# Kernel tuning notes

Hardware: AMD Instinct MI355X
Metric: run time of the kernel (lower is better)

The kernel has to match this reference:

```python
import jax, jax.numpy as jnp
import numpy as np

EPS = 1e-08
F_DIM = 512


def setup_inputs() -> dict:
    key = jax.random.key(0)
    ks = jax.random.split(key, 7)
    N, F = 50000, F_DIM
    q = jax.random.normal(ks[0], (N, 1, F), dtype=jnp.float32)
    mu = jax.random.normal(ks[1], (N, 3, F), dtype=jnp.float32)
    # Xavier-ish scaled params
    W_mix = jax.random.normal(ks[2], (2 * F, F), dtype=jnp.float32) * (1.0 / np.sqrt(F))
    W1 = jax.random.normal(ks[3], (F, 2 * F), dtype=jnp.float32) * (1.0 / np.sqrt(2 * F))
    b1 = jnp.zeros((F,), dtype=jnp.float32)
    W2 = jax.random.normal(ks[4], (3 * F, F), dtype=jnp.float32) * (1.0 / np.sqrt(F))
    b2 = jnp.zeros((3 * F,), dtype=jnp.float32)
    return {"q": q, "mu": mu, "W_mix": W_mix, "W1": W1, "b1": b1, "W2": W2, "b2": b2}


def reference(q, mu, W_mix, W1, b1, W2, b2):
    F = q.shape[-1]
    # mu_channel_mix: [N,3,F] @ [F,2F] -> [N,3,2F]
    mu_mix = jnp.einsum('ndf,gf->ndg', mu, W_mix)
    mu_V, mu_W = mu_mix[..., :F], mu_mix[..., F:]
    # vector norm over Cartesian axis -> [N,1,F]
    mu_Vn = jnp.sqrt(jnp.sum(mu_V * mu_V, axis=-2, keepdims=True) + EPS)
    ctx = jnp.concatenate([q, mu_Vn], axis=-1)  # [N,1,2F]
    h = jax.nn.silu(jnp.einsum('nsf,gf->nsg', ctx, W1) + b1)  # [N,1,F]
    x = jnp.einsum('nsf,gf->nsg', h, W2) + b2  # [N,1,3F]
    dq_intra = x[..., :F]
    dmu_intra = x[..., F:2 * F] * mu_W  # broadcast [N,1,F]*[N,3,F]
    dqmu_intra = x[..., 2 * F:] * jnp.sum(mu_V * mu_W, axis=1, keepdims=True)
    q_out = q + dq_intra + dqmu_intra
    mu_out = mu + dmu_intra
    return (q_out, mu_out)
```

## Files before the change

kernel.cpp:

```cpp
#include <hip/hip_runtime.h>
#include <stdint.h>

#define NN 50000
#define QWORDS 25600000

typedef __attribute__((ext_vector_type(8))) short bf16x8;
typedef __attribute__((ext_vector_type(4))) float f32x4;

__device__ __forceinline__ uint32_t f2bf(float x){
  uint32_t u = __builtin_bit_cast(uint32_t, x);
  u += 0x7FFFu + ((u >> 16) & 1u);
  return u >> 16;
}
__device__ __forceinline__ float bf2f(uint32_t b){
  uint32_t u = b << 16;
  return __builtin_bit_cast(float, u);
}
__device__ __forceinline__ void gload16(const uint16_t* g, uint16_t* l){
  __builtin_amdgcn_global_load_lds(
      (const __attribute__((address_space(1))) uint32_t*)g,
      (__attribute__((address_space(3))) uint32_t*)l, 16, 0, 0);
}
__device__ __forceinline__ f32x4 mfma16(bf16x8 a, bf16x8 b, f32x4 c){
  return __builtin_amdgcn_mfma_f32_16x16x32_bf16(a, b, c, 0, 0, 0);
}

#define FENCE() asm volatile("" ::: "memory")

__global__ void k_convert(const float* __restrict__ wmix, const float* __restrict__ w1,
                          const float* __restrict__ w2, uint16_t* __restrict__ dst){
  int i = blockIdx.x * 256 + threadIdx.x;
  int e = i << 2;
  const float* s; int o;
  if (e < 524288)       { s = wmix; o = e; }
  else if (e < 1048576) { s = w1;   o = e - 524288; }
  else                  { s = w2;   o = e - 1048576; }
  f32x4 v = *(const f32x4*)(s + o);
  uint2 pk;
  pk.x = f2bf(v[0]) | (f2bf(v[1]) << 16);
  pk.y = f2bf(v[2]) | (f2bf(v[3]) << 16);
  *(uint2*)(dst + e) = pk;
}

__global__ void k_convmu(const float* __restrict__ mu, uint16_t* __restrict__ dst){
  size_t i = (size_t)blockIdx.x * 256 + threadIdx.x;
  size_t e = i << 2;
  f32x4 v = *(const f32x4*)(mu + e);
  uint2 pk;
  pk.x = f2bf(v[0]) | (f2bf(v[1]) << 16);
  pk.y = f2bf(v[2]) | (f2bf(v[3]) << 16);
  *(uint2*)(dst + e) = pk;
}

__global__ __launch_bounds__(512, 4)
void k_gemm1(const float* __restrict__ mu, const uint16_t* __restrict__ wmixb,
             uint16_t* __restrict__ qh, float* __restrict__ muW){
  __shared__ uint16_t As[2][12288];
  __shared__ uint16_t Bs[2][8192];
  const int tid  = threadIdx.x;
  const int lane = tid & 63;
  const int w    = tid >> 6;
  const int wn   = w & 3;
  const int wf   = w >> 2;
  const int orig = blockIdx.x;
  const int j    = (orig & 7) * 782 + (orig >> 3);
  const int f0   = (j & 7) * 64;
  const int n0   = (j >> 3) * 64;
  const int lrow = tid >> 4;
  const int lcol = (tid & 15) * 4;

  f32x4 ar[6];
  auto A_LOAD = [&](int ks){
    const int k0 = ks * 64;
    #pragma unroll
    for (int p=0; p<6; ++p){
      int r = p*32 + lrow;
      int d = r >> 6, nrow = r & 63;
      int n = n0 + nrow;
      int g = (n < NN ? n : NN-1)*3 + d;
      ar[p] = *(const f32x4*)(mu + (size_t)g*512 + k0 + lcol);
    }
  };
  auto A_WRITE = [&](int buf){
    #pragma unroll
    for (int p=0; p<6; ++p){
      int r = p*32 + lrow;
      f32x4 v = ar[p];
      uint2 pk;
      pk.x = f2bf(v[0]) | (f2bf(v[1]) << 16);
      pk.y = f2bf(v[2]) | (f2bf(v[3]) << 16);
      *(uint2*)&As[buf][r*64 + (lcol ^ ((r&7)<<3))] = pk;
    }
  };
  auto B_ISSUE = [&](int ks, int buf){
    const int k0 = ks * 64;
    #pragma unroll
    for (int jj=0; jj<2; ++jj){
      int jb = w*2 + jj;
      int row = jb*8 + (lane>>3);
      int g = (row < 64) ? (f0 + row) : (448 + f0 + row);
      int srcc = ((lane&7) ^ ((lane>>3)&7)) * 8;
      gload16(wmixb + (size_t)g*512 + k0 + srcc, &Bs[buf][jb*512]);
    }
  };

  const f32x4 z4 = {0.f,0.f,0.f,0.f};
  f32x4 acc[3][4];
  #pragma unroll
  for (int d=0; d<3; ++d)
    #pragma unroll
    for (int nt=0; nt<4; ++nt) acc[d][nt] = z4;

  A_LOAD(0); B_ISSUE(0, 0); A_WRITE(0);
  for (int ks=0; ks<8; ++ks){
    const int cur = ks & 1;
    __syncthreads();
    if (ks < 7){ A_LOAD(ks+1); B_ISSUE(ks+1, cur^1); }
    #pragma unroll
    for (int kf=0; kf<2; ++kf){
      int kc = kf*32 + (lane>>4)*8;
      bf16x8 af[3];
      #pragma unroll
      for (int d=0; d<3; ++d){
        int r = d*64 + wn*16 + (lane&15);
        af[d] = *(const bf16x8*)&As[cur][r*64 + (kc ^ ((r&7)<<3))];
      }
      #pragma unroll
      for (int nt=0; nt<4; ++nt){
        int ntg = wf*2 + (nt&1) + (nt>>1)*4;
        int rr = ntg*16 + (lane&15);
        bf16x8 bf = *(const bf16x8*)&Bs[cur][rr*64 + (kc ^ ((rr&7)<<3))];
        #pragma unroll
        for (int d=0; d<3; ++d)
          acc[d][nt] = mfma16(bf, af[d], acc[d][nt]);
      }
    }
    if (ks < 7) A_WRITE(cur^1);
  }

  const int rb4 = (lane >> 4) * 4;
  const int nthr = n0 + wn*16 + (lane & 15);
  if (nthr < NN){
    #pragma unroll
    for (int c=0; c<2; ++c){
      int f = f0 + (wf*2 + c)*16 + rb4;
      uint2 pkv, pkd; f32x4 u0v, u1v, u2v;
      uint32_t vb[4], db[4];
      #pragma unroll
      for (int p=0; p<4; ++p){
        float v0 = acc[0][c][p],   v1 = acc[1][c][p],   v2 = acc[2][c][p];
        float u0 = acc[0][c+2][p], u1 = acc[1][c+2][p], u2 = acc[2][c+2][p];
        float vn = sqrtf(v0*v0 + v1*v1 + v2*v2 + 1e-8f);
        float dt = v0*u0 + v1*u1 + v2*u2;
        vb[p] = f2bf(vn); db[p] = f2bf(dt);
        u0v[p] = u0; u1v[p] = u1; u2v[p] = u2;
      }
      pkv.x = vb[0] | (vb[1] << 16); pkv.y = vb[2] | (vb[3] << 16);
      pkd.x = db[0] | (db[1] << 16); pkd.y = db[2] | (db[3] << 16);
      *(uint2*)(qh + (size_t)nthr*1024 + f)       = pkv;
      *(uint2*)(qh + (size_t)nthr*1024 + 512 + f) = pkd;
      size_t mb = (size_t)nthr*1536 + f;
      *(f32x4*)(muW + mb)        = u0v;
      *(f32x4*)(muW + mb + 512)  = u1v;
      *(f32x4*)(muW + mb + 1024) = u2v;
    }
  }
}

__global__ __launch_bounds__(512, 4)
void k_gemm1b(const uint16_t* __restrict__ mu16, const uint16_t* __restrict__ wmixb,
              uint16_t* __restrict__ qh, float* __restrict__ muW){
  __shared__ uint16_t As[2][12288];
  __shared__ uint16_t Bs[2][8192];
  const int tid  = threadIdx.x;
  const int lane = tid & 63;
  const int w    = tid >> 6;
  const int wn   = w & 3;
  const int wf   = w >> 2;
  const int orig = blockIdx.x;
  const int j    = (orig & 7) * 782 + (orig >> 3);
  const int f0   = (j & 7) * 64;
  const int n0   = (j >> 3) * 64;

  auto A_ISSUE = [&](int ks, int buf){
    const int k0 = ks * 64;
    #pragma unroll
    for (int jj=0; jj<3; ++jj){
      int jb = w*3 + jj;
      int rr = jb*8 + (lane>>3);
      int d = rr >> 6, nrow = rr & 63;
      int n = n0 + nrow;
      int g = (n < NN ? n : NN-1)*3 + d;
      int srcc = ((lane&7) ^ ((lane>>3)&7)) * 8;
      gload16(mu16 + (size_t)g*512 + k0 + srcc, &As[buf][jb*512]);
    }
  };
  auto B_ISSUE = [&](int ks, int buf){
    const int k0 = ks * 64;
    #pragma unroll
    for (int jj=0; jj<2; ++jj){
      int jb = w*2 + jj;
      int row = jb*8 + (lane>>3);
      int g = (row < 64) ? (f0 + row) : (448 + f0 + row);
      int srcc = ((lane&7) ^ ((lane>>3)&7)) * 8;
      gload16(wmixb + (size_t)g*512 + k0 + srcc, &Bs[buf][jb*512]);
    }
  };

  const f32x4 z4 = {0.f,0.f,0.f,0.f};
  f32x4 acc[3][4];
  #pragma unroll
  for (int d=0; d<3; ++d)
    #pragma unroll
    for (int nt=0; nt<4; ++nt) acc[d][nt] = z4;

  A_ISSUE(0, 0); B_ISSUE(0, 0);
  for (int ks=0; ks<8; ++ks){
    const int cur = ks & 1;
    __syncthreads();
    if (ks < 7){ A_ISSUE(ks+1, cur^1); B_ISSUE(ks+1, cur^1); }
    #pragma unroll
    for (int kf=0; kf<2; ++kf){
      int kc = kf*32 + (lane>>4)*8;
      bf16x8 af[3];
      #pragma unroll
      for (int d=0; d<3; ++d){
        int r = d*64 + wn*16 + (lane&15);
        af[d] = *(const bf16x8*)&As[cur][r*64 + (kc ^ ((r&7)<<3))];
      }
      #pragma unroll
      for (int nt=0; nt<4; ++nt){
        int ntg = wf*2 + (nt&1) + (nt>>1)*4;
        int rr = ntg*16 + (lane&15);
        bf16x8 bf = *(const bf16x8*)&Bs[cur][rr*64 + (kc ^ ((rr&7)<<3))];
        #pragma unroll
        for (int d=0; d<3; ++d)
          acc[d][nt] = mfma16(bf, af[d], acc[d][nt]);
      }
    }
  }

  const int rb4 = (lane >> 4) * 4;
  const int nthr = n0 + wn*16 + (lane & 15);
  if (nthr < NN){
    #pragma unroll
    for (int c=0; c<2; ++c){
      int f = f0 + (wf*2 + c)*16 + rb4;
      uint2 pkv, pkd; f32x4 u0v, u1v, u2v;
      uint32_t vb[4], db[4];
      #pragma unroll
      for (int p=0; p<4; ++p){
        float v0 = acc[0][c][p],   v1 = acc[1][c][p],   v2 = acc[2][c][p];
        float u0 = acc[0][c+2][p], u1 = acc[1][c+2][p], u2 = acc[2][c+2][p];
        float vn = sqrtf(v0*v0 + v1*v1 + v2*v2 + 1e-8f);
        float dt = v0*u0 + v1*u1 + v2*u2;
        vb[p] = f2bf(vn); db[p] = f2bf(dt);
        u0v[p] = u0; u1v[p] = u1; u2v[p] = u2;
      }
      pkv.x = vb[0] | (vb[1] << 16); pkv.y = vb[2] | (vb[3] << 16);
      pkd.x = db[0] | (db[1] << 16); pkd.y = db[2] | (db[3] << 16);
      *(uint2*)(qh + (size_t)nthr*1024 + f)       = pkv;
      *(uint2*)(qh + (size_t)nthr*1024 + 512 + f) = pkd;
      size_t mb = (size_t)nthr*1536 + f;
      *(f32x4*)(muW + mb)        = u0v;
      *(f32x4*)(muW + mb + 512)  = u1v;
      *(f32x4*)(muW + mb + 1024) = u2v;
    }
  }
}

__global__ __launch_bounds__(512, 4)
void k_gemm2(const float* __restrict__ q, const uint16_t* __restrict__ w1b,
             const float* __restrict__ b1, uint16_t* __restrict__ qh){
  __shared__ uint16_t A2[2][2048];
  __shared__ uint16_t B2[2][16384];
  const int tid  = threadIdx.x;
  const int lane = tid & 63;
  const int w    = tid >> 6;
  const int wm   = w >> 2;
  const int wn   = w & 3;
  const int n0   = blockIdx.x * 64;

  f32x4 qa;
  auto QA_LOAD = [&](int s){
    int k0 = s*32;
    int row = tid >> 3, ch = tid & 7;
    int nc = (n0 + row < NN) ? n0 + row : NN-1;
    qa = *(const f32x4*)(q + (size_t)nc*512 + k0 + ch*4);
  };
  auto QA_WRITE = [&](int buf){
    int row = tid >> 3, ch = tid & 7;
    uint2 pk;
    pk.x = f2bf(qa[0]) | (f2bf(qa[1]) << 16);
    pk.y = f2bf(qa[2]) | (f2bf(qa[3]) << 16);
    *(uint2*)&A2[buf][row*32 + (((ch>>1) ^ (row&3))<<3) + (ch&1)*4] = pk;
  };
  auto VA_ISSUE = [&](int s, int buf){
    if (w < 4){
      int k0v = (s-16)*32;
      int row = w*16 + (lane>>2);
      int nc = (n0 + row < NN) ? n0 + row : NN-1;
      int srcch = (lane&3) ^ (row&3);
      gload16(qh + (size_t)nc*1024 + k0v + srcch*8, &A2[buf][w*512]);
    }
  };
  auto B_ISSUE = [&](int s, int buf){
    int k0 = s*32;
    #pragma unroll
    for (int jj=0; jj<4; ++jj){
      int j = w*4 + jj;
      int row = j*16 + (lane>>2);
      int srcch = (lane&3) ^ (row&3);
      gload16(w1b + (size_t)row*1024 + k0 + srcch*8, &B2[buf][j*512]);
    }
  };

  const f32x4 z4 = {0.f,0.f,0.f,0.f};
  f32x4 acc2[2][8];
  #pragma unroll
  for (int mt=0; mt<2; ++mt)
    #pragma unroll
    for (int nt=0; nt<8; ++nt) acc2[mt][nt] = z4;

  QA_LOAD(0); B_ISSUE(0, 0); QA_WRITE(0);
  for (int s=0; s<32; ++s){
    const int cur = s & 1;
    __syncthreads();
    if (s < 31){
      if (s+1 < 16) QA_LOAD(s+1); else VA_ISSUE(s+1, cur^1);
      B_ISSUE(s+1, cur^1);
    }
    {
      int kc = (lane>>4)*8;
      bf16x8 a[2];
      #pragma unroll
      for (int mt=0; mt<2; ++mt){
        int r = wm*32 + mt*16 + (lane&15);
        a[mt] = *(const bf16x8*)&A2[cur][r*32 + (kc ^ ((r&3)<<3))];
      }
      #pragma unroll
      for (int nt=0; nt<8; ++nt){
        int rr = wn*128 + nt*16 + (lane&15);
        bf16x8 b = *(const bf16x8*)&B2[cur][rr*32 + (kc ^ ((rr&3)<<3))];
        acc2[0][nt] = mfma16(a[0], b, acc2[0][nt]);
        acc2[1][nt] = mfma16(a[1], b, acc2[1][nt]);
      }
    }
    if (s < 31 && s+1 < 16) QA_WRITE(cur^1);
  }

  const int rb4 = (lane >> 4) * 4;
  #pragma unroll
  for (int nt=0; nt<8; ++nt){
    int col = wn*128 + nt*16 + (lane&15);
    float bb = b1[col];
    #pragma unroll
    for (int mt=0; mt<2; ++mt)
      #pragma unroll
      for (int j=0; j<4; ++j){
        int n = n0 + wm*32 + mt*16 + rb4 + j;
        if (n < NN){
          float x = acc2[mt][nt][j] + bb;
          float sv = x / (1.f + __expf(-x));
          qh[(size_t)n*1024 + col] = (uint16_t)f2bf(sv);
        }
      }
  }
}

__global__ __launch_bounds__(512, 4)
void k_gemm3(const float* __restrict__ q, const float* __restrict__ mu,
             const uint16_t* __restrict__ w2b, const float* __restrict__ b2,
             float* __restrict__ dout){
  __shared__ uint16_t Hs[32*512];
  __shared__ uint16_t B3[2][12288];
  const int tid  = threadIdx.x;
  const int lane = tid & 63;
  const int w    = tid >> 6;
  const int wm   = w >> 2;
  const int wn   = w & 3;
  const int n0   = blockIdx.x * 32;
  const uint16_t* qh = (const uint16_t*)dout;
  float* mout = dout + (size_t)QWORDS;
  const int l15 = lane & 15;
  const int rb4 = (lane >> 4) * 4;
  const f32x4 z4 = {0.f,0.f,0.f,0.f};

  #pragma unroll
  for (int i=0; i<4; ++i){
    int row = w*4 + i;
    int nc = (n0 + row < NN) ? n0 + row : NN-1;
    gload16(qh + (size_t)nc*1024 + (size_t)((lane ^ (row&7))*8), &Hs[row*512]);
  }

  auto B_ISSUE = [&](int it, int ks, uint16_t* slot){
    #pragma unroll
    for (int jj=0; jj<3; ++jj){
      int j = w*3 + jj;
      int rr = j*8 + (lane>>3);
      int s3 = rr >> 6, fi = rr & 63;
      int g = s3*512 + it*64 + fi;
      gload16(w2b + (size_t)g*512 + ks*64 + ((lane&7) ^ (rr&7))*8, slot + j*512);
    }
  };
  B_ISSUE(0, 0, B3[0]);

  const int nthr = n0 + wm*16 + l15;
  const int nc   = nthr < NN ? nthr : NN-1;

  f32x4 qv, bbv[3], muv[3], mwv[3];
  float dtv[4];
  int   fb = 0;
  f32x4 acc3[3];

#define K3_MFMA(KS) do{ \
    const uint16_t* bsl = B3[(KS)&1]; \
    __builtin_amdgcn_s_setprio(1); \
    _Pragma("unroll") \
    for (int kf=0; kf<2; ++kf){ \
      int r = wm*16 + l15; \
      int ch = ((KS)*8 + kf*4 + (lane>>4)) ^ (r&7); \
      bf16x8 a = *(const bf16x8*)&Hs[r*512 + ch*8]; \
      _Pragma("unroll") \
      for (int s3=0; s3<3; ++s3){ \
        int rr = s3*64 + wn*16 + l15; \
        int chb = (kf*4 + (lane>>4)) ^ (rr&7); \
        bf16x8 b = *(const bf16x8*)&bsl[rr*64 + chb*8]; \
        acc3[s3] = mfma16(b, a, acc3[s3]); \
      } \
    } \
    __builtin_amdgcn_s_setprio(0); \
  } while(0)

  #pragma unroll 1
  for (int it=0; it<8; ++it){
    if (it) { asm volatile("s_waitcnt vmcnt(4)" ::: "memory"); }
    else    { asm volatile("s_waitcnt vmcnt(0)" ::: "memory"); }
    __builtin_amdgcn_s_barrier();
    B_ISSUE(it, 1, B3[1]);
    FENCE();
    {
      #pragma unroll
      for (int s3=0; s3<3; ++s3) acc3[s3] = z4;
      fb = it*64 + wn*16 + rb4;
      bbv[0] = *(const f32x4*)(b2 + fb);
      bbv[1] = *(const f32x4*)(b2 + 512 + fb);
      bbv[2] = *(const f32x4*)(b2 + 1024 + fb);
      uint2 du = *(const uint2*)(qh + (size_t)nc*1024 + 512 + fb);
      dtv[0] = bf2f(du.x & 0xffff); dtv[1] = bf2f(du.x >> 16);
      dtv[2] = bf2f(du.y & 0xffff); dtv[3] = bf2f(du.y >> 16);
      qv = *(const f32x4*)(q + (size_t)nc*512 + fb);
    }
    FENCE();
    K3_MFMA(0);

    asm volatile("s_waitcnt vmcnt(5)" ::: "memory");
    __builtin_amdgcn_s_barrier();
    B_ISSUE(it, 2, B3[0]);
    FENCE();
    {
      size_t mb = (size_t)nc*1536 + fb;
      muv[0] = *(const f32x4*)(mu + mb);
      muv[1] = *(const f32x4*)(mu + mb + 512);
      muv[2] = *(const f32x4*)(mu + mb + 1024);
    }
    FENCE();
    K3_MFMA(1);

    asm volatile("s_waitcnt vmcnt(3)" ::: "memory");
    __builtin_amdgcn_s_barrier();
    B_ISSUE(it, 3, B3[1]);
    FENCE();
    {
      size_t mb = (size_t)nc*1536 + fb;
      mwv[0] = *(const f32x4*)(mout + mb);
      mwv[1] = *(const f32x4*)(mout + mb + 512);
      mwv[2] = *(const f32x4*)(mout + mb + 1024);
    }
    FENCE();
    K3_MFMA(2);

    asm volatile("s_waitcnt vmcnt(3)" ::: "memory");
    __builtin_amdgcn_s_barrier();
    B_ISSUE(it, 4, B3[0]);
    FENCE();
    K3_MFMA(3);

    asm volatile("s_waitcnt vmcnt(0)" ::: "memory");
    __builtin_amdgcn_s_barrier();
    B_ISSUE(it, 5, B3[1]);
    FENCE();
    K3_MFMA(4);

    asm volatile("s_waitcnt vmcnt(0)" ::: "memory");
    __builtin_amdgcn_s_barrier();
    B_ISSUE(it, 6, B3[0]);
    FENCE();
    K3_MFMA(5);

    asm volatile("s_waitcnt vmcnt(0)" ::: "memory");
    __builtin_amdgcn_s_barrier();
    B_ISSUE(it, 7, B3[1]);
    FENCE();
    K3_MFMA(6);

    asm volatile("s_waitcnt vmcnt(0)" ::: "memory");
    __builtin_amdgcn_s_barrier();
    if (it < 7) B_ISSUE(it+1, 0, B3[0]);
    FENCE();
    K3_MFMA(7);
    if (nthr < NN){
      f32x4 qo, m0, m1, m2;
      #pragma unroll
      for (int p=0; p<4; ++p){
        float x0 = acc3[0][p] + bbv[0][p];
        float x1 = acc3[1][p] + bbv[1][p];
        float x2 = acc3[2][p] + bbv[2][p];
        qo[p] = qv[p] + x0 + x2*dtv[p];
        m0[p] = muv[0][p] + x1*mwv[0][p];
        m1[p] = muv[1][p] + x1*mwv[1][p];
        m2[p] = muv[2][p] + x1*mwv[2][p];
      }
      *(f32x4*)(dout + (size_t)nthr*512 + fb) = qo;
      size_t mb = (size_t)nthr*1536 + fb;
      *(f32x4*)(mout + mb)        = m0;
      *(f32x4*)(mout + mb + 512)  = m1;
      *(f32x4*)(mout + mb + 1024) = m2;
    }
  }
#undef K3_MFMA
}

extern "C" void kernel_launch(void* const* d_in, const int* in_sizes, int n_in,
                              void* d_out, int out_size, void* d_ws, size_t ws_size,
                              hipStream_t stream){
  (void)in_sizes; (void)n_in; (void)out_size;
  const float* q    = (const float*)d_in[0];
  const float* mu   = (const float*)d_in[1];
  const float* wmix = (const float*)d_in[2];
  const float* w1   = (const float*)d_in[3];
  const float* b1   = (const float*)d_in[4];
  const float* w2   = (const float*)d_in[5];
  const float* b2   = (const float*)d_in[6];
  uint16_t* wb = (uint16_t*)d_ws;
  float* dout = (float*)d_out;

  hipLaunchKernelGGL(k_convert, dim3(1792), dim3(256), 0, stream, wmix, w1, w2, wb);

  const size_t need = ((size_t)1835008 + (size_t)NN*1536) * 2;
  if (ws_size >= need){
    uint16_t* mu16 = wb + 1835008;
    hipLaunchKernelGGL(k_convmu, dim3(75000), dim3(256), 0, stream, mu, mu16);
    hipLaunchKernelGGL(k_gemm1b, dim3(6256), dim3(512), 0, stream,
                       mu16, wb, (uint16_t*)d_out, dout + (size_t)QWORDS);
  } else {
    hipLaunchKernelGGL(k_gemm1, dim3(6256), dim3(512), 0, stream,
                       mu, wb, (uint16_t*)d_out, dout + (size_t)QWORDS);
  }

  hipLaunchKernelGGL(k_gemm2, dim3(782), dim3(512), 0, stream,
                     q, wb + 524288, b1, (uint16_t*)d_out);
  hipLaunchKernelGGL(k_gemm3, dim3(1563), dim3(512), 0, stream,
                     q, mu, wb + 1048576, b2, dout);
}
```

Measured before the change: 916.3 us.

## Fuse mu bf16 conversion into gemm1 and store mu_W intermediate as bf16

```diff
diff --git a/kernel.cpp b/kernel.cpp
--- a/kernel.cpp
+++ b/kernel.cpp
@@ -36,16 +36,6 @@
   else if (e < 1048576) { s = w1;   o = e - 524288; }
   else                  { s = w2;   o = e - 1048576; }
   f32x4 v = *(const f32x4*)(s + o);
-  uint2 pk;
-  pk.x = f2bf(v[0]) | (f2bf(v[1]) << 16);
-  pk.y = f2bf(v[2]) | (f2bf(v[3]) << 16);
-  *(uint2*)(dst + e) = pk;
-}
-
-__global__ void k_convmu(const float* __restrict__ mu, uint16_t* __restrict__ dst){
-  size_t i = (size_t)blockIdx.x * 256 + threadIdx.x;
-  size_t e = i << 2;
-  f32x4 v = *(const f32x4*)(mu + e);
   uint2 pk;
   pk.x = f2bf(v[0]) | (f2bf(v[1]) << 16);
   pk.y = f2bf(v[2]) | (f2bf(v[3]) << 16);
@@ -168,8 +158,8 @@
 }
 
 __global__ __launch_bounds__(512, 4)
-void k_gemm1b(const uint16_t* __restrict__ mu16, const uint16_t* __restrict__ wmixb,
-              uint16_t* __restrict__ qh, float* __restrict__ muW){
+void k_gemm1b(const float* __restrict__ mu, const uint16_t* __restrict__ wmixb,
+              uint16_t* __restrict__ qh, uint16_t* __restrict__ mw16){
   __shared__ uint16_t As[2][12288];
   __shared__ uint16_t Bs[2][8192];
   const int tid  = threadIdx.x;
@@ -181,18 +171,30 @@
   const int j    = (orig & 7) * 782 + (orig >> 3);
   const int f0   = (j & 7) * 64;
   const int n0   = (j >> 3) * 64;
-
-  auto A_ISSUE = [&](int ks, int buf){
+  const int lrow = tid >> 4;
+  const int lcol = (tid & 15) * 4;
+
+  f32x4 ar[6];
+  auto A_LOAD = [&](int ks){
     const int k0 = ks * 64;
     #pragma unroll
-    for (int jj=0; jj<3; ++jj){
-      int jb = w*3 + jj;
-      int rr = jb*8 + (lane>>3);
-      int d = rr >> 6, nrow = rr & 63;
+    for (int p=0; p<6; ++p){
+      int r = p*32 + lrow;
+      int d = r >> 6, nrow = r & 63;
       int n = n0 + nrow;
       int g = (n < NN ? n : NN-1)*3 + d;
-      int srcc = ((lane&7) ^ ((lane>>3)&7)) * 8;
-      gload16(mu16 + (size_t)g*512 + k0 + srcc, &As[buf][jb*512]);
+      ar[p] = *(const f32x4*)(mu + (size_t)g*512 + k0 + lcol);
+    }
+  };
+  auto A_WRITE = [&](int buf){
+    #pragma unroll
+    for (int p=0; p<6; ++p){
+      int r = p*32 + lrow;
+      f32x4 v = ar[p];
+      uint2 pk;
+      pk.x = f2bf(v[0]) | (f2bf(v[1]) << 16);
+      pk.y = f2bf(v[2]) | (f2bf(v[3]) << 16);
+      *(uint2*)&As[buf][r*64 + (lcol ^ ((r&7)<<3))] = pk;
     }
   };
   auto B_ISSUE = [&](int ks, int buf){
@@ -214,11 +216,11 @@
     #pragma unroll
     for (int nt=0; nt<4; ++nt) acc[d][nt] = z4;
 
-  A_ISSUE(0, 0); B_ISSUE(0, 0);
+  A_LOAD(0); B_ISSUE(0, 0); A_WRITE(0);
   for (int ks=0; ks<8; ++ks){
     const int cur = ks & 1;
     __syncthreads();
-    if (ks < 7){ A_ISSUE(ks+1, cur^1); B_ISSUE(ks+1, cur^1); }
+    if (ks < 7){ A_LOAD(ks+1); B_ISSUE(ks+1, cur^1); }
     #pragma unroll
     for (int kf=0; kf<2; ++kf){
       int kc = kf*32 + (lane>>4)*8;
@@ -238,6 +240,7 @@
           acc[d][nt] = mfma16(bf, af[d], acc[d][nt]);
       }
     }
+    if (ks < 7) A_WRITE(cur^1);
   }
 
   const int rb4 = (lane >> 4) * 4;
@@ -246,8 +249,8 @@
     #pragma unroll
     for (int c=0; c<2; ++c){
       int f = f0 + (wf*2 + c)*16 + rb4;
-      uint2 pkv, pkd; f32x4 u0v, u1v, u2v;
-      uint32_t vb[4], db[4];
+      uint2 pkv, pkd, pw0, pw1, pw2;
+      uint32_t vb[4], db[4], w0[4], w1[4], w2[4];
       #pragma unroll
       for (int p=0; p<4; ++p){
         float v0 = acc[0][c][p],   v1 = acc[1][c][p],   v2 = acc[2][c][p];
@@ -255,16 +258,19 @@
         float vn = sqrtf(v0*v0 + v1*v1 + v2*v2 + 1e-8f);
         float dt = v0*u0 + v1*u1 + v2*u2;
         vb[p] = f2bf(vn); db[p] = f2bf(dt);
-        u0v[p] = u0; u1v[p] = u1; u2v[p] = u2;
+        w0[p] = f2bf(u0); w1[p] = f2bf(u1); w2[p] = f2bf(u2);
       }
       pkv.x = vb[0] | (vb[1] << 16); pkv.y = vb[2] | (vb[3] << 16);
       pkd.x = db[0] | (db[1] << 16); pkd.y = db[2] | (db[3] << 16);
+      pw0.x = w0[0] | (w0[1] << 16); pw0.y = w0[2] | (w0[3] << 16);
+      pw1.x = w1[0] | (w1[1] << 16); pw1.y = w1[2] | (w1[3] << 16);
+      pw2.x = w2[0] | (w2[1] << 16); pw2.y = w2[2] | (w2[3] << 16);
       *(uint2*)(qh + (size_t)nthr*1024 + f)       = pkv;
       *(uint2*)(qh + (size_t)nthr*1024 + 512 + f) = pkd;
       size_t mb = (size_t)nthr*1536 + f;
-      *(f32x4*)(muW + mb)        = u0v;
-      *(f32x4*)(muW + mb + 512)  = u1v;
-      *(f32x4*)(muW + mb + 1024) = u2v;
+      *(uint2*)(mw16 + mb)        = pw0;
+      *(uint2*)(mw16 + mb + 512)  = pw1;
+      *(uint2*)(mw16 + mb + 1024) = pw2;
     }
   }
 }
@@ -368,50 +374,127 @@
   }
 }
 
-__global__ __launch_bounds__(512, 4)
-void k_gemm3(const float* __restrict__ q, const float* __restrict__ mu,
-             const uint16_t* __restrict__ w2b, const float* __restrict__ b2,
-             float* __restrict__ dout){
-  __shared__ uint16_t Hs[32*512];
-  __shared__ uint16_t B3[2][12288];
-  const int tid  = threadIdx.x;
-  const int lane = tid & 63;
-  const int w    = tid >> 6;
-  const int wm   = w >> 2;
-  const int wn   = w & 3;
-  const int n0   = blockIdx.x * 32;
-  const uint16_t* qh = (const uint16_t*)dout;
-  float* mout = dout + (size_t)QWORDS;
-  const int l15 = lane & 15;
-  const int rb4 = (lane >> 4) * 4;
-  const f32x4 z4 = {0.f,0.f,0.f,0.f};
-
-  #pragma unroll
-  for (int i=0; i<4; ++i){
-    int row = w*4 + i;
-    int nc = (n0 + row < NN) ? n0 + row : NN-1;
-    gload16(qh + (size_t)nc*1024 + (size_t)((lane ^ (row&7))*8), &Hs[row*512]);
-  }
-
-  auto B_ISSUE = [&](int it, int ks, uint16_t* slot){
-    #pragma unroll
-    for (int jj=0; jj<3; ++jj){
-      int j = w*3 + jj;
-      int rr = j*8 + (lane>>3);
-      int s3 = rr >> 6, fi = rr & 63;
-      int g = s3*512 + it*64 + fi;
-      gload16(w2b + (size_t)g*512 + ks*64 + ((lane&7) ^ (rr&7))*8, slot + j*512);
-    }
-  };
-  B_ISSUE(0, 0, B3[0]);
-
-  const int nthr = n0 + wm*16 + l15;
-  const int nc   = nthr < NN ? nthr : NN-1;
-
-  f32x4 qv, bbv[3], muv[3], mwv[3];
-  float dtv[4];
-  int   fb = 0;
-  f32x4 acc3[3];
+#define K3_BODY(MW_LOAD_STMT)                                                  \
+  __shared__ uint16_t Hs[32*512];                                    \
+  __shared__ uint16_t B3[2][12288];                           \
+  const int tid  = threadIdx.x;                                                \
+  const int lane = tid & 63;                                                   \
+  const int w    = tid >> 6;                                                   \
+  const int wm   = w >> 2;                                                     \
+  const int wn   = w & 3;                                                      \
+  const int n0   = blockIdx.x * 32;                                            \
+  const uint16_t* qh = (const uint16_t*)dout;                                  \
+  float* mout = dout + (size_t)QWORDS;                                         \
+  const int l15 = lane & 15;                                                   \
+  const int rb4 = (lane >> 4) * 4;                                             \
+  const f32x4 z4 = {0.f,0.f,0.f,0.f};                                          \
+  _Pragma("unroll")                                                            \
+  for (int i=0; i<4; ++i){                                                     \
+    int row = w*4 + i;                                                         \
+    int nc2 = (n0 + row < NN) ? n0 + row : NN-1;                               \
+    gload16(qh + (size_t)nc2*1024 + (size_t)((lane ^ (row&7))*8), &Hs[row*512]);\
+  }                                                                            \
+  auto B_ISSUE = [&](int it, int ks, uint16_t* slot){                          \
+    _Pragma("unroll")                                                          \
+    for (int jj=0; jj<3; ++jj){                                                \
+      int jx = w*3 + jj;                                                       \
+      int rr = jx*8 + (lane>>3);                                               \
+      int s3 = rr >> 6, fi = rr & 63;                                          \
+      int g = s3*512 + it*64 + fi;                                             \
+      gload16(w2b + (size_t)g*512 + ks*64 + ((lane&7) ^ (rr&7))*8, slot + jx*512);\
+    }                                                                          \
+  };                                                                           \
+  B_ISSUE(0, 0, B3[0]);                                                        \
+  const int nthr = n0 + wm*16 + l15;                                           \
+  const int nc   = nthr < NN ? nthr : NN-1;                                    \
+  f32x4 qv, bbv[3], muv[3], mwv[3];                                            \
+  float dtv[4];                                                                \
+  int   fb = 0;                                                                \
+  f32x4 acc3[3];                                                               \
+  _Pragma("unroll 1")                                                          \
+  for (int it=0; it<8; ++it){                                                  \
+    if (it) { asm volatile("s_waitcnt vmcnt(4)" ::: "memory"); }               \
+    else    { asm volatile("s_waitcnt vmcnt(0)" ::: "memory"); }               \
+    __builtin_amdgcn_s_barrier();                                              \
+    B_ISSUE(it, 1, B3[1]);                                                     \
+    FENCE();                                                                   \
+    {                                                                          \
+      _Pragma("unroll")                                                        \
+      for (int s3=0; s3<3; ++s3) acc3[s3] = z4;                                \
+      fb = it*64 + wn*16 + rb4;                                                \
+      bbv[0] = *(const f32x4*)(b2 + fb);                                       \
+      bbv[1] = *(const f32x4*)(b2 + 512 + fb);                                 \
+      bbv[2] = *(const f32x4*)(b2 + 1024 + fb);                                \
+      uint2 du = *(const uint2*)(qh + (size_t)nc*1024 + 512 + fb);             \
+      dtv[0] = bf2f(du.x & 0xffff); dtv[1] = bf2f(du.x >> 16);                 \
+      dtv[2] = bf2f(du.y & 0xffff); dtv[3] = bf2f(du.y >> 16);                 \
+      qv = *(const f32x4*)(q + (size_t)nc*512 + fb);                           \
+    }                                                                          \
+    FENCE();                                                                   \
+    K3_MFMA(0);                                                                \
+    asm volatile("s_waitcnt vmcnt(5)" ::: "memory");                           \
+    __builtin_amdgcn_s_barrier();                                              \
+    B_ISSUE(it, 2, B3[0]);                                                     \
+    FENCE();                                                                   \
+    {                                                                          \
+      size_t mb = (size_t)nc*1536 + fb;                                        \
+      muv[0] = *(const f32x4*)(mu + mb);                                       \
+      muv[1] = *(const f32x4*)(mu + mb + 512);                                 \
+      muv[2] = *(const f32x4*)(mu + mb + 1024);                                \
+    }                                                                          \
+    FENCE();                                                                   \
+    K3_MFMA(1);                                                                \
+    asm volatile("s_waitcnt vmcnt(3)" ::: "memory");                           \
+    __builtin_amdgcn_s_barrier();                                              \
+    B_ISSUE(it, 3, B3[1]);                                                     \
+    FENCE();                                                                   \
+    { MW_LOAD_STMT }                                                           \
+    FENCE();                                                                   \
+    K3_MFMA(2);                                                                \
+    asm volatile("s_waitcnt vmcnt(3)" ::: "memory");                           \
+    __builtin_amdgcn_s_barrier();                                              \
+    B_ISSUE(it, 4, B3[0]);                                                     \
+    FENCE();                                                                   \
+    K3_MFMA(3);                                                                \
+    asm volatile("s_waitcnt vmcnt(0)" ::: "memory");                           \
+    __builtin_amdgcn_s_barrier();                                              \
+    B_ISSUE(it, 5, B3[1]);                                                     \
+    FENCE();                                                                   \
+    K3_MFMA(4);                                                                \
+    asm volatile("s_waitcnt vmcnt(0)" ::: "memory");                           \
+    __builtin_amdgcn_s_barrier();                                              \
+    B_ISSUE(it, 6, B3[0]);                                                     \
+    FENCE();                                                                   \
+    K3_MFMA(5);                                                                \
+    asm volatile("s_waitcnt vmcnt(0)" ::: "memory");                           \
+    __builtin_amdgcn_s_barrier();                                              \
+    B_ISSUE(it, 7, B3[1]);                                                     \
+    FENCE();                                                                   \
+    K3_MFMA(6);                                                                \
+    asm volatile("s_waitcnt vmcnt(0)" ::: "memory");                           \
+    __builtin_amdgcn_s_barrier();                                              \
+    if (it < 7) B_ISSUE(it+1, 0, B3[0]);                                       \
+    FENCE();                                                                   \
+    K3_MFMA(7);                                                                \
+    if (nthr < NN){                                                            \
+      f32x4 qo, m0, m1, m2;                                                    \
+      _Pragma("unroll")                                                        \
+      for (int p=0; p<4; ++p){                                                 \
+        float x0 = acc3[0][p] + bbv[0][p];                                     \
+        float x1 = acc3[1][p] + bbv[1][p];                                     \
+        float x2 = acc3[2][p] + bbv[2][p];                                     \
+        qo[p] = qv[p] + x0 + x2*dtv[p];                                        \
+        m0[p] = muv[0][p] + x1*mwv[0][p];                                      \
+        m1[p] = muv[1][p] + x1*mwv[1][p];                                      \
+        m2[p] = muv[2][p] + x1*mwv[2][p];                                      \
+      }                                                                        \
+      *(f32x4*)(dout + (size_t)nthr*512 + fb) = qo;                            \
+      size_t mb = (size_t)nthr*1536 + fb;                                      \
+      *(f32x4*)(mout + mb)        = m0;                                        \
+      *(f32x4*)(mout + mb + 512)  = m1;                                        \
+      *(f32x4*)(mout + mb + 1024) = m2;                                        \
+    }                                                                          \
+  }
 
 #define K3_MFMA(KS) do{ \
     const uint16_t* bsl = B3[(KS)&1]; \
@@ -432,103 +515,34 @@
     __builtin_amdgcn_s_setprio(0); \
   } while(0)
 
-  #pragma unroll 1
-  for (int it=0; it<8; ++it){
-    if (it) { asm volatile("s_waitcnt vmcnt(4)" ::: "memory"); }
-    else    { asm volatile("s_waitcnt vmcnt(0)" ::: "memory"); }
-    __builtin_amdgcn_s_barrier();
-    B_ISSUE(it, 1, B3[1]);
-    FENCE();
-    {
-      #pragma unroll
-      for (int s3=0; s3<3; ++s3) acc3[s3] = z4;
-      fb = it*64 + wn*16 + rb4;
-      bbv[0] = *(const f32x4*)(b2 + fb);
-      bbv[1] = *(const f32x4*)(b2 + 512 + fb);
-      bbv[2] = *(const f32x4*)(b2 + 1024 + fb);
-      uint2 du = *(const uint2*)(qh + (size_t)nc*1024 + 512 + fb);
-      dtv[0] = bf2f(du.x & 0xffff); dtv[1] = bf2f(du.x >> 16);
-      dtv[2] = bf2f(du.y & 0xffff); dtv[3] = bf2f(du.y >> 16);
-      qv = *(const f32x4*)(q + (size_t)nc*512 + fb);
-    }
-    FENCE();
-    K3_MFMA(0);
-
-    asm volatile("s_waitcnt vmcnt(5)" ::: "memory");
-    __builtin_amdgcn_s_barrier();
-    B_ISSUE(it, 2, B3[0]);
-    FENCE();
-    {
-      size_t mb = (size_t)nc*1536 + fb;
-      muv[0] = *(const f32x4*)(mu + mb);
-      muv[1] = *(const f32x4*)(mu + mb + 512);
-      muv[2] = *(const f32x4*)(mu + mb + 1024);
-    }
-    FENCE();
-    K3_MFMA(1);
-
-    asm volatile("s_waitcnt vmcnt(3)" ::: "memory");
-    __builtin_amdgcn_s_barrier();
-    B_ISSUE(it, 3, B3[1]);
-    FENCE();
-    {
+__global__ __launch_bounds__(512, 4)
+void k_gemm3(const float* __restrict__ q, const float* __restrict__ mu,
+             const uint16_t* __restrict__ w2b, const float* __restrict__ b2,
+             float* __restrict__ dout){
+  K3_BODY(
       size_t mb = (size_t)nc*1536 + fb;
       mwv[0] = *(const f32x4*)(mout + mb);
       mwv[1] = *(const f32x4*)(mout + mb + 512);
       mwv[2] = *(const f32x4*)(mout + mb + 1024);
-    }
-    FENCE();
-    K3_MFMA(2);
-
-    asm volatile("s_waitcnt vmcnt(3)" ::: "memory");
-    __builtin_amdgcn_s_barrier();
-    B_ISSUE(it, 4, B3[0]);
-    FENCE();
-    K3_MFMA(3);
-
-    asm volatile("s_waitcnt vmcnt(0)" ::: "memory");
-    __builtin_amdgcn_s_barrier();
-    B_ISSUE(it, 5, B3[1]);
-    FENCE();
-    K3_MFMA(4);
-
-    asm volatile("s_waitcnt vmcnt(0)" ::: "memory");
-    __builtin_amdgcn_s_barrier();
-    B_ISSUE(it, 6, B3[0]);
-    FENCE();
-    K3_MFMA(5);
-
-    asm volatile("s_waitcnt vmcnt(0)" ::: "memory");
-    __builtin_amdgcn_s_barrier();
-    B_ISSUE(it, 7, B3[1]);
-    FENCE();
-    K3_MFMA(6);
-
-    asm volatile("s_waitcnt vmcnt(0)" ::: "memory");
-    __builtin_amdgcn_s_barrier();
-    if (it < 7) B_ISSUE(it+1, 0, B3[0]);
-    FENCE();
-    K3_MFMA(7);
-    if (nthr < NN){
-      f32x4 qo, m0, m1, m2;
-      #pragma unroll
-      for (int p=0; p<4; ++p){
-        float x0 = acc3[0][p] + bbv[0][p];
-        float x1 = acc3[1][p] + bbv[1][p];
-        float x2 = acc3[2][p] + bbv[2][p];
-        qo[p] = qv[p] + x0 + x2*dtv[p];
-        m0[p] = muv[0][p] + x1*mwv[0][p];
-        m1[p] = muv[1][p] + x1*mwv[1][p];
-        m2[p] = muv[2][p] + x1*mwv[2][p];
-      }
-      *(f32x4*)(dout + (size_t)nthr*512 + fb) = qo;
-      size_t mb = (size_t)nthr*1536 + fb;
-      *(f32x4*)(mout + mb)        = m0;
-      *(f32x4*)(mout + mb + 512)  = m1;
-      *(f32x4*)(mout + mb + 1024) = m2;
-    }
-  }
-#undef K3_MFMA
+  )
+}
+
+__global__ __launch_bounds__(512, 4)
+void k_gemm3b(const float* __restrict__ q, const float* __restrict__ mu,
+              const uint16_t* __restrict__ w2b, const float* __restrict__ b2,
+              float* __restrict__ dout, const uint16_t* __restrict__ mw16){
+  K3_BODY(
+      size_t mb = (size_t)nc*1536 + fb;
+      uint2 a0 = *(const uint2*)(mw16 + mb);
+      uint2 a1 = *(const uint2*)(mw16 + mb + 512);
+      uint2 a2 = *(const uint2*)(mw16 + mb + 1024);
+      mwv[0][0]=bf2f(a0.x&0xffff); mwv[0][1]=bf2f(a0.x>>16);
+      mwv[0][2]=bf2f(a0.y&0xffff); mwv[0][3]=bf2f(a0.y>>16);
+      mwv[1][0]=bf2f(a1.x&0xffff); mwv[1][1]=bf2f(a1.x>>16);
+      mwv[1][2]=bf2f(a1.y&0xffff); mwv[1][3]=bf2f(a1.y>>16);
+      mwv[2][0]=bf2f(a2.x&0xffff); mwv[2][1]=bf2f(a2.x>>16);
+      mwv[2][2]=bf2f(a2.y&0xffff); mwv[2][3]=bf2f(a2.y>>16);
+  )
 }
 
 extern "C" void kernel_launch(void* const* d_in, const int* in_sizes, int n_in,
@@ -549,17 +563,19 @@
 
   const size_t need = ((size_t)1835008 + (size_t)NN*1536) * 2;
   if (ws_size >= need){
-    uint16_t* mu16 = wb + 1835008;
-    hipLaunchKernelGGL(k_convmu, dim3(75000), dim3(256), 0, stream, mu, mu16);
+    uint16_t* mw16 = wb + 1835008;
     hipLaunchKernelGGL(k_gemm1b, dim3(6256), dim3(512), 0, stream,
-                       mu16, wb, (uint16_t*)d_out, dout + (size_t)QWORDS);
+                       mu, wb, (uint16_t*)d_out, mw16);
+    hipLaunchKernelGGL(k_gemm2, dim3(782), dim3(512), 0, stream,
+                       q, wb + 524288, b1, (uint16_t*)d_out);
+    hipLaunchKernelGGL(k_gemm3b, dim3(1563), dim3(512), 0, stream,
+                       q, mu, wb + 1048576, b2, dout, mw16);
   } else {
     hipLaunchKernelGGL(k_gemm1, dim3(6256), dim3(512), 0, stream,
                        mu, wb, (uint16_t*)d_out, dout + (size_t)QWORDS);
-  }
-
-  hipLaunchKernelGGL(k_gemm2, dim3(782), dim3(512), 0, stream,
-                     q, wb + 524288, b1, (uint16_t*)d_out);
-  hipLaunchKernelGGL(k_gemm3, dim3(1563), dim3(512), 0, stream,
-                     q, mu, wb + 1048576, b2, dout);
-}
+    hipLaunchKernelGGL(k_gemm2, dim3(782), dim3(512), 0, stream,
+                       q, wb + 524288, b1, (uint16_t*)d_out);
+    hipLaunchKernelGGL(k_gemm3, dim3(1563), dim3(512), 0, stream,
+                       q, mu, wb + 1048576, b2, dout);
+  }
+}
```

Result: faster. 861.3 us (-6.0%).

## Fuse mu bf16 conversion into gemm1, store mu_W as bf16 workspace, add smaller-tile gemm3

Applied to the files above, without the earlier changes.

```diff
diff --git a/kernel.cpp b/kernel.cpp
--- a/kernel.cpp
+++ b/kernel.cpp
@@ -36,16 +36,6 @@
   else if (e < 1048576) { s = w1;   o = e - 524288; }
   else                  { s = w2;   o = e - 1048576; }
   f32x4 v = *(const f32x4*)(s + o);
-  uint2 pk;
-  pk.x = f2bf(v[0]) | (f2bf(v[1]) << 16);
-  pk.y = f2bf(v[2]) | (f2bf(v[3]) << 16);
-  *(uint2*)(dst + e) = pk;
-}
-
-__global__ void k_convmu(const float* __restrict__ mu, uint16_t* __restrict__ dst){
-  size_t i = (size_t)blockIdx.x * 256 + threadIdx.x;
-  size_t e = i << 2;
-  f32x4 v = *(const f32x4*)(mu + e);
   uint2 pk;
   pk.x = f2bf(v[0]) | (f2bf(v[1]) << 16);
   pk.y = f2bf(v[2]) | (f2bf(v[3]) << 16);
@@ -168,8 +158,8 @@
 }
 
 __global__ __launch_bounds__(512, 4)
-void k_gemm1b(const uint16_t* __restrict__ mu16, const uint16_t* __restrict__ wmixb,
-              uint16_t* __restrict__ qh, float* __restrict__ muW){
+void k_gemm1b(const float* __restrict__ mu, const uint16_t* __restrict__ wmixb,
+              uint16_t* __restrict__ qh, uint16_t* __restrict__ mw16){
   __shared__ uint16_t As[2][12288];
   __shared__ uint16_t Bs[2][8192];
   const int tid  = threadIdx.x;
@@ -181,18 +171,30 @@
   const int j    = (orig & 7) * 782 + (orig >> 3);
   const int f0   = (j & 7) * 64;
   const int n0   = (j >> 3) * 64;
-
-  auto A_ISSUE = [&](int ks, int buf){
+  const int lrow = tid >> 4;
+  const int lcol = (tid & 15) * 4;
+
+  f32x4 ar[6];
+  auto A_LOAD = [&](int ks){
     const int k0 = ks * 64;
     #pragma unroll
-    for (int jj=0; jj<3; ++jj){
-      int jb = w*3 + jj;
-      int rr = jb*8 + (lane>>3);
-      int d = rr >> 6, nrow = rr & 63;
+    for (int p=0; p<6; ++p){
+      int r = p*32 + lrow;
+      int d = r >> 6, nrow = r & 63;
       int n = n0 + nrow;
       int g = (n < NN ? n : NN-1)*3 + d;
-      int srcc = ((lane&7) ^ ((lane>>3)&7)) * 8;
-      gload16(mu16 + (size_t)g*512 + k0 + srcc, &As[buf][jb*512]);
+      ar[p] = *(const f32x4*)(mu + (size_t)g*512 + k0 + lcol);
+    }
+  };
+  auto A_WRITE = [&](int buf){
+    #pragma unroll
+    for (int p=0; p<6; ++p){
+      int r = p*32 + lrow;
+      f32x4 v = ar[p];
+      uint2 pk;
+      pk.x = f2bf(v[0]) | (f2bf(v[1]) << 16);
+      pk.y = f2bf(v[2]) | (f2bf(v[3]) << 16);
+      *(uint2*)&As[buf][r*64 + (lcol ^ ((r&7)<<3))] = pk;
     }
   };
   auto B_ISSUE = [&](int ks, int buf){
@@ -214,11 +216,11 @@
     #pragma unroll
     for (int nt=0; nt<4; ++nt) acc[d][nt] = z4;
 
-  A_ISSUE(0, 0); B_ISSUE(0, 0);
+  A_LOAD(0); B_ISSUE(0, 0); A_WRITE(0);
   for (int ks=0; ks<8; ++ks){
     const int cur = ks & 1;
     __syncthreads();
-    if (ks < 7){ A_ISSUE(ks+1, cur^1); B_ISSUE(ks+1, cur^1); }
+    if (ks < 7){ A_LOAD(ks+1); B_ISSUE(ks+1, cur^1); }
     #pragma unroll
     for (int kf=0; kf<2; ++kf){
       int kc = kf*32 + (lane>>4)*8;
@@ -238,6 +240,7 @@
           acc[d][nt] = mfma16(bf, af[d], acc[d][nt]);
       }
     }
+    if (ks < 7) A_WRITE(cur^1);
   }
 
   const int rb4 = (lane >> 4) * 4;
@@ -246,8 +249,8 @@
     #pragma unroll
     for (int c=0; c<2; ++c){
       int f = f0 + (wf*2 + c)*16 + rb4;
-      uint2 pkv, pkd; f32x4 u0v, u1v, u2v;
-      uint32_t vb[4], db[4];
+      uint2 pkv, pkd, pw0, pw1, pw2;
+      uint32_t vb[4], db[4], w0[4], w1[4], w2[4];
       #pragma unroll
       for (int p=0; p<4; ++p){
         float v0 = acc[0][c][p],   v1 = acc[1][c][p],   v2 = acc[2][c][p];
@@ -255,16 +258,19 @@
         float vn = sqrtf(v0*v0 + v1*v1 + v2*v2 + 1e-8f);
         float dt = v0*u0 + v1*u1 + v2*u2;
         vb[p] = f2bf(vn); db[p] = f2bf(dt);
-        u0v[p] = u0; u1v[p] = u1; u2v[p] = u2;
+        w0[p] = f2bf(u0); w1[p] = f2bf(u1); w2[p] = f2bf(u2);
       }
       pkv.x = vb[0] | (vb[1] << 16); pkv.y = vb[2] | (vb[3] << 16);
       pkd.x = db[0] | (db[1] << 16); pkd.y = db[2] | (db[3] << 16);
+      pw0.x = w0[0] | (w0[1] << 16); pw0.y = w0[2] | (w0[3] << 16);
+      pw1.x = w1[0] | (w1[1] << 16); pw1.y = w1[2] | (w1[3] << 16);
+      pw2.x = w2[0] | (w2[1] << 16); pw2.y = w2[2] | (w2[3] << 16);
       *(uint2*)(qh + (size_t)nthr*1024 + f)       = pkv;
       *(uint2*)(qh + (size_t)nthr*1024 + 512 + f) = pkd;
       size_t mb = (size_t)nthr*1536 + f;
-      *(f32x4*)(muW + mb)        = u0v;
-      *(f32x4*)(muW + mb + 512)  = u1v;
-      *(f32x4*)(muW + mb + 1024) = u2v;
+      *(uint2*)(mw16 + mb)        = pw0;
+      *(uint2*)(mw16 + mb + 512)  = pw1;
+      *(uint2*)(mw16 + mb + 1024) = pw2;
     }
   }
 }
@@ -366,6 +372,170 @@
         }
       }
   }
+}
+
+__global__ __launch_bounds__(256, 4)
+void k_gemm3c(const float* __restrict__ q, const float* __restrict__ mu,
+              const uint16_t* __restrict__ w2b, const float* __restrict__ b2,
+              float* __restrict__ dout, const uint16_t* __restrict__ mw16){
+  __shared__ uint16_t Hs[16*512];
+  __shared__ uint16_t B3[2][6144];
+  const int tid  = threadIdx.x;
+  const int lane = tid & 63;
+  const int w    = tid >> 6;
+  const int n0   = blockIdx.x * 16;
+  const uint16_t* qh = (const uint16_t*)dout;
+  float* mout = dout + (size_t)QWORDS;
+  const int l15 = lane & 15;
+  const int rb4 = (lane >> 4) * 4;
+  const f32x4 z4 = {0.f,0.f,0.f,0.f};
+
+  #pragma unroll
+  for (int i=0; i<4; ++i){
+    int row = w*4 + i;
+    int nc2 = (n0 + row < NN) ? n0 + row : NN-1;
+    gload16(qh + (size_t)nc2*1024 + (size_t)((lane ^ (row&7))*8), &Hs[row*512]);
+  }
+
+  auto B_ISSUE = [&](int it, int ks, uint16_t* slot){
+    #pragma unroll
+    for (int jj=0; jj<3; ++jj){
+      int j = w*3 + jj;
+      int rr = j*16 + (lane>>2);
+      int s3 = rr >> 6, fi = rr & 63;
+      int g = s3*512 + it*64 + fi;
+      int srcc = ((lane&3) ^ (rr&3)) * 8;
+      gload16(w2b + (size_t)g*512 + ks*32 + srcc, slot + j*512);
+    }
+  };
+  B_ISSUE(0, 0, B3[0]);
+
+  const int nthr = n0 + l15;
+  const int nc   = nthr < NN ? nthr : NN-1;
+
+  f32x4 qv, bbv[3], muv[3], mwv[3];
+  float dtv[4];
+  int   fb = 0;
+  f32x4 acc3[3];
+
+#define K3C_MFMA(P) do{ \
+    const uint16_t* bsl = B3[(P)&1]; \
+    __builtin_amdgcn_s_setprio(1); \
+    { \
+      int r = l15; \
+      int ch = ((P)*4 + (lane>>4)) ^ (r&7); \
+      bf16x8 a = *(const bf16x8*)&Hs[r*512 + ch*8]; \
+      _Pragma("unroll") \
+      for (int s3=0; s3<3; ++s3){ \
+        int rr = s3*64 + w*16 + l15; \
+        int chb = (lane>>4) ^ (rr&3); \
+        bf16x8 b = *(const bf16x8*)&bsl[rr*32 + chb*8]; \
+        acc3[s3] = mfma16(b, a, acc3[s3]); \
+      } \
+    } \
+    __builtin_amdgcn_s_setprio(0); \
+  } while(0)
+
+#define K3C_PHASE(P, WAIT) \
+    asm volatile("s_waitcnt vmcnt(" #WAIT ")" ::: "memory"); \
+    __builtin_amdgcn_s_barrier(); \
+    B_ISSUE(it, (P)+1, B3[((P)+1)&1]); \
+    FENCE(); \
+    K3C_MFMA(P);
+
+  #pragma unroll 1
+  for (int it=0; it<8; ++it){
+    if (it) { asm volatile("s_waitcnt vmcnt(4)" ::: "memory"); }
+    else    { asm volatile("s_waitcnt vmcnt(0)" ::: "memory"); }
+    __builtin_amdgcn_s_barrier();
+    B_ISSUE(it, 1, B3[1]);
+    FENCE();
+    {
+      #pragma unroll
+      for (int s3=0; s3<3; ++s3) acc3[s3] = z4;
+      fb = it*64 + w*16 + rb4;
+      bbv[0] = *(const f32x4*)(b2 + fb);
+      bbv[1] = *(const f32x4*)(b2 + 512 + fb);
+      bbv[2] = *(const f32x4*)(b2 + 1024 + fb);
+      uint2 du = *(const uint2*)(qh + (size_t)nc*1024 + 512 + fb);
+      dtv[0] = bf2f(du.x & 0xffff); dtv[1] = bf2f(du.x >> 16);
+      dtv[2] = bf2f(du.y & 0xffff); dtv[3] = bf2f(du.y >> 16);
+      qv = *(const f32x4*)(q + (size_t)nc*512 + fb);
+    }
+    FENCE();
+    K3C_MFMA(0);
+
+    asm volatile("s_waitcnt vmcnt(5)" ::: "memory");
+    __builtin_amdgcn_s_barrier();
+    B_ISSUE(it, 2, B3[0]);
+    FENCE();
+    {
+      size_t mb = (size_t)nc*1536 + fb;
+      muv[0] = *(const f32x4*)(mu + mb);
+      muv[1] = *(const f32x4*)(mu + mb + 512);
+      muv[2] = *(const f32x4*)(mu + mb + 1024);
+    }
+    FENCE();
+    K3C_MFMA(1);
+
+    asm volatile("s_waitcnt vmcnt(3)" ::: "memory");
+    __builtin_amdgcn_s_barrier();
+    B_ISSUE(it, 3, B3[1]);
+    FENCE();
+    {
+      size_t mb = (size_t)nc*1536 + fb;
+      uint2 a0 = *(const uint2*)(mw16 + mb);
+      uint2 a1 = *(const uint2*)(mw16 + mb + 512);
+      uint2 a2 = *(const uint2*)(mw16 + mb + 1024);
+      mwv[0][0]=bf2f(a0.x&0xffff); mwv[0][1]=bf2f(a0.x>>16);
+      mwv[0][2]=bf2f(a0.y&0xffff); mwv[0][3]=bf2f(a0.y>>16);
+      mwv[1][0]=bf2f(a1.x&0xffff); mwv[1][1]=bf2f(a1.x>>16);
+      mwv[1][2]=bf2f(a1.y&0xffff); mwv[1][3]=bf2f(a1.y>>16);
+      mwv[2][0]=bf2f(a2.x&0xffff); mwv[2][1]=bf2f(a2.x>>16);
+      mwv[2][2]=bf2f(a2.y&0xffff); mwv[2][3]=bf2f(a2.y>>16);
+    }
+    FENCE();
+    K3C_MFMA(2);
+
+    K3C_PHASE(3, 3)
+    K3C_PHASE(4, 0)
+    K3C_PHASE(5, 0)
+    K3C_PHASE(6, 0)
+    K3C_PHASE(7, 0)
+    K3C_PHASE(8, 0)
+    K3C_PHASE(9, 0)
+    K3C_PHASE(10, 0)
+    K3C_PHASE(11, 0)
+    K3C_PHASE(12, 0)
+    K3C_PHASE(13, 0)
+    K3C_PHASE(14, 0)
+
+    asm volatile("s_waitcnt vmcnt(0)" ::: "memory");
+    __builtin_amdgcn_s_barrier();
+    if (it < 7) B_ISSUE(it+1, 0, B3[0]);
+    FENCE();
+    K3C_MFMA(15);
+    if (nthr < NN){
+      f32x4 qo, m0, m1, m2;
+      #pragma unroll
+      for (int p=0; p<4; ++p){
+        float x0 = acc3[0][p] + bbv[0][p];
+        float x1 = acc3[1][p] + bbv[1][p];
+        float x2 = acc3[2][p] + bbv[2][p];
+        qo[p] = qv[p] + x0 + x2*dtv[p];
+        m0[p] = muv[0][p] + x1*mwv[0][p];
+        m1[p] = muv[1][p] + x1*mwv[1][p];
+        m2[p] = muv[2][p] + x1*mwv[2][p];
+      }
+      *(f32x4*)(dout + (size_t)nthr*512 + fb) = qo;
+      size_t mb = (size_t)nthr*1536 + fb;
+      *(f32x4*)(mout + mb)        = m0;
+      *(f32x4*)(mout + mb + 512)  = m1;
+      *(f32x4*)(mout + mb + 1024) = m2;
+    }
+  }
+#undef K3C_PHASE
+#undef K3C_MFMA
 }
 
 __global__ __launch_bounds__(512, 4)
@@ -389,18 +559,18 @@
   #pragma unroll
   for (int i=0; i<4; ++i){
     int row = w*4 + i;
-    int nc = (n0 + row < NN) ? n0 + row : NN-1;
-    gload16(qh + (size_t)nc*1024 + (size_t)((lane ^ (row&7))*8), &Hs[row*512]);
+    int nc2 = (n0 + row < NN) ? n0 + row : NN-1;
+    gload16(qh + (size_t)nc2*1024 + (size_t)((lane ^ (row&7))*8), &Hs[row*512]);
   }
 
   auto B_ISSUE = [&](int it, int ks, uint16_t* slot){
     #pragma unroll
     for (int jj=0; jj<3; ++jj){
-      int j = w*3 + jj;
-      int rr = j*8 + (lane>>3);
+      int jx = w*3 + jj;
+      int rr = jx*8 + (lane>>3);
       int s3 = rr >> 6, fi = rr & 63;
       int g = s3*512 + it*64 + fi;
-      gload16(w2b + (size_t)g*512 + ks*64 + ((lane&7) ^ (rr&7))*8, slot + j*512);
+      gload16(w2b + (size_t)g*512 + ks*64 + ((lane&7) ^ (rr&7))*8, slot + jx*512);
     }
   };
   B_ISSUE(0, 0, B3[0]);
@@ -549,17 +719,19 @@
 
   const size_t need = ((size_t)1835008 + (size_t)NN*1536) * 2;
   if (ws_size >= need){
-    uint16_t* mu16 = wb + 1835008;
-    hipLaunchKernelGGL(k_convmu, dim3(75000), dim3(256), 0, stream, mu, mu16);
+    uint16_t* mw16 = wb + 1835008;
     hipLaunchKernelGGL(k_gemm1b, dim3(6256), dim3(512), 0, stream,
-                       mu16, wb, (uint16_t*)d_out, dout + (size_t)QWORDS);
+                       mu, wb, (uint16_t*)d_out, mw16);
+    hipLaunchKernelGGL(k_gemm2, dim3(782), dim3(512), 0, stream,
+                       q, wb + 524288, b1, (uint16_t*)d_out);
+    hipLaunchKernelGGL(k_gemm3c, dim3(3125), dim3(256), 0, stream,
+                       q, mu, wb + 1048576, b2, dout, mw16);
   } else {
     hipLaunchKernelGGL(k_gemm1, dim3(6256), dim3(512), 0, stream,
                        mu, wb, (uint16_t*)d_out, dout + (size_t)QWORDS);
-  }
-
-  hipLaunchKernelGGL(k_gemm2, dim3(782), dim3(512), 0, stream,
-                     q, wb + 524288, b1, (uint16_t*)d_out);
-  hipLaunchKernelGGL(k_gemm3, dim3(1563), dim3(512), 0, stream,
-                     q, mu, wb + 1048576, b2, dout);
-}
+    hipLaunchKernelGGL(k_gemm2, dim3(782), dim3(512), 0, stream,
+                       q, wb + 524288, b1, (uint16_t*)d_out);
+    hipLaunchKernelGGL(k_gemm3, dim3(1563), dim3(512), 0, stream,
+                       q, mu, wb + 1048576, b2, dout);
+  }
+}
```

Result: slower. 972.7 us (+6.2%).
